# Optimization experiments

Measured on AMD Instinct MI355X. Metric: run time of the kernel, lower is better.

Reference implementation:

```python
import jax, jax.numpy as jnp
import numpy as np

EPS = 1e-12  # matches torch F.normalize default eps
TEMP = 0.1


def _gram(x):
    # L2-normalize rows; for unit vectors 1 - 0.5*||xi-xj||^2 == xi . xj
    n = x / jnp.maximum(jnp.linalg.norm(x, axis=-1, keepdims=True), EPS)
    return n @ n.T  # [N, N]


def setup_inputs() -> dict:
    key = jax.random.key(0)
    k1, k2, k3, k4 = jax.random.split(key, 4)
    N, D = 4096, 512
    return {
        "fm_rgb": jax.random.normal(k1, (N, D), dtype=jnp.float32),
        "fm_depth": jax.random.normal(k2, (N, D), dtype=jnp.float32),
        "fm_ir": jax.random.normal(k3, (N, D), dtype=jnp.float32),
        "fm_t": jax.random.normal(k4, (N, D), dtype=jnp.float32),
    }


def reference(fm_rgb, fm_depth, fm_ir, fm_t):
    G_rgb = _gram(fm_rgb)
    G_depth = _gram(fm_depth)
    G_ir = _gram(fm_ir)
    G_t = _gram(fm_t)
    inv_t = 1.0 / TEMP
    loss_rgb = jnp.mean((G_t * inv_t - G_rgb * inv_t) ** 2)
    loss_depth = jnp.mean((G_t * inv_t - G_depth * inv_t) ** 2)
    loss_ir = jnp.mean((G_t * inv_t - G_ir * inv_t) ** 2)
    return loss_rgb + loss_depth + loss_ir
```

## Files before the change

kernel.cpp:

```cpp
#include <hip/hip_runtime.h>
#include <hip/hip_bf16.h>


typedef __attribute__((ext_vector_type(4))) float floatx4;
typedef __attribute__((ext_vector_type(2))) long long llx2;

#define N_ROWS 4096
#define DDIM   512
#define LOSS_SCALE 9.094947017729282e-11f

__device__ __forceinline__ const float* sel_mod(int mod, const float* a,
                                                const float* b, const float* c,
                                                const float* d) {
  return mod == 0 ? a : mod == 1 ? b : mod == 2 ? c : d;
}

__device__ __forceinline__ float bfr(float x) {
  __hip_bfloat16 h = __float2bfloat16(x);
  unsigned short u = *(unsigned short*)&h;
  return __uint_as_float(((unsigned int)u) << 16);
}

__global__ __launch_bounds__(256) void preprocess_kernel(
    const float* __restrict__ in0, const float* __restrict__ in1,
    const float* __restrict__ in2, const float* __restrict__ in3,
    unsigned char* __restrict__ nT8, float* __restrict__ out) {
  int mod = blockIdx.y;
  int k0 = blockIdx.x * 32;
  const float* X = sel_mod(mod, in0, in1, in2, in3) + (size_t)k0 * DDIM;

  if (blockIdx.x == 0 && blockIdx.y == 0 && threadIdx.x == 0)
    out[0] = 0.f;

  __shared__ float rsc[32];
  __shared__ unsigned int t8[128 * 9];

  int t = threadIdx.x;
  int w = t >> 6, lane = t & 63;

#pragma unroll
  for (int i = 0; i < 8; ++i) {
    int r = w * 8 + i;
    const float4* rp = (const float4*)(X + (size_t)r * DDIM);
    float4 a = rp[lane];
    float4 b = rp[lane + 64];
    float ss = a.x * a.x + a.y * a.y + a.z * a.z + a.w * a.w +
               b.x * b.x + b.y * b.y + b.z * b.z + b.w * b.w;
#pragma unroll
    for (int off = 32; off > 0; off >>= 1) ss += __shfl_down(ss, off, 64);
    if (lane == 0) rsc[r] = 16.0f / fmaxf(sqrtf(ss), 1e-12f);
  }
  __syncthreads();

  int ag = t >> 5;
  int bg = t & 31;
  float sc[4];
#pragma unroll
  for (int q = 0; q < 4; ++q) sc[q] = rsc[ag * 4 + q];

  for (int p = 0; p < 4; ++p) {
    float4 v[4];
#pragma unroll
    for (int q = 0; q < 4; ++q)
      v[q] = ((const float4*)(X + (size_t)(ag * 4 + q) * DDIM + p * 128))[bg];
#pragma unroll
    for (int j = 0; j < 4; ++j) {
      float f0 = bfr(((const float*)&v[0])[j] * sc[0]);
      float f1 = bfr(((const float*)&v[1])[j] * sc[1]);
      float f2 = bfr(((const float*)&v[2])[j] * sc[2]);
      float f3 = bfr(((const float*)&v[3])[j] * sc[3]);
      unsigned int pk = __builtin_amdgcn_cvt_pk_fp8_f32(f0, f1, 0, 0);
      pk = __builtin_amdgcn_cvt_pk_fp8_f32(f2, f3, pk, 1);
      t8[(bg * 4 + j) * 9 + ag] = pk;
    }
    __syncthreads();
    {
      int col = t >> 1, g = t & 1;
      uint4 o;
      o.x = t8[col * 9 + g * 4 + 0];
      o.y = t8[col * 9 + g * 4 + 1];
      o.z = t8[col * 9 + g * 4 + 2];
      o.w = t8[col * 9 + g * 4 + 3];
      *(uint4*)(nT8 + ((size_t)(mod * DDIM + p * 128 + col)) * N_ROWS + k0 +
                g * 16) = o;
    }
    __syncthreads();
  }
}

__device__ __forceinline__ void stage_tiles(
    const unsigned char* __restrict__ Abase,
    const unsigned char* __restrict__ Bbase, int k0,
    unsigned char* ls, int w, int lane) {
  int rr = lane >> 3;
  int s = lane & 7;
#pragma unroll
  for (int c = 0; c < 2; ++c) {
    int base = c * 32 + w * 8;
    int row = base + rr;
    int gc = s ^ ((row >> 1) & 7);
    const unsigned char* ga = Abase + (size_t)row * N_ROWS + k0 + gc * 16;
    __builtin_amdgcn_global_load_lds(
        (__attribute__((address_space(1))) void*)(void*)ga,
        (__attribute__((address_space(3))) void*)(void*)&ls[base * 128],
        16, 0, 0);
  }
#pragma unroll
  for (int c = 0; c < 2; ++c) {
    int base = c * 32 + w * 8;
    int row = base + rr;
    int gc = s ^ ((row >> 1) & 7);
    const unsigned char* gb = Bbase + (size_t)row * N_ROWS + k0 + gc * 16;
    __builtin_amdgcn_global_load_lds(
        (__attribute__((address_space(1))) void*)(void*)gb,
        (__attribute__((address_space(3))) void*)(void*)&ls[8192 + base * 128],
        16, 0, 0);
  }
}

__device__ __forceinline__ void compute_tiles(
    const unsigned char* ls, floatx4 acc[2][2], int wm, int wn, int lm,
    int lq) {
  llx2 A16[2][2], B16[2][2];
#pragma unroll
  for (int mi = 0; mi < 2; ++mi) {
    int row = wm + mi * 16 + lm;
    int sw = (row >> 1) & 7;
    A16[mi][0] = *(const llx2*)&ls[row * 128 + ((lq * 2) ^ sw) * 16];
    A16[mi][1] = *(const llx2*)&ls[row * 128 + ((lq * 2 + 1) ^ sw) * 16];
  }
#pragma unroll
  for (int ni = 0; ni < 2; ++ni) {
    int row = wn + ni * 16 + lm;
    int sw = (row >> 1) & 7;
    B16[ni][0] = *(const llx2*)&ls[8192 + row * 128 + ((lq * 2) ^ sw) * 16];
    B16[ni][1] =
        *(const llx2*)&ls[8192 + row * 128 + ((lq * 2 + 1) ^ sw) * 16];
  }
#pragma unroll
  for (int ks = 0; ks < 4; ++ks) {
    int h = ks >> 1, e = ks & 1;
#pragma unroll
    for (int mi = 0; mi < 2; ++mi)
#pragma unroll
      for (int ni = 0; ni < 2; ++ni)
        acc[mi][ni] = __builtin_amdgcn_mfma_f32_16x16x32_fp8_fp8(
            A16[mi][h][e], B16[ni][h][e], acc[mi][ni], 0, 0, 0);
  }
}

__global__ __launch_bounds__(256) void gram_frob_kernel(
    const unsigned char* __restrict__ nT8, float* __restrict__ out) {
  __shared__ __align__(16) unsigned char ls[2][16384];
  __shared__ float red[4];

  int bx = blockIdx.x;
  int pa_, pb_, ti, tj;
  float wgt;
  if (bx < 144) {
    int p = bx / 36;
    int t36 = bx - p * 36;
    int i = 0;
    while (t36 >= 8 - i) { t36 -= 8 - i; ++i; }
    ti = i;
    tj = i + t36;
    const int   sm[4] = {3, 0, 1, 2};
    const float sw_[4] = {3.f, 1.f, 1.f, 1.f};
    pa_ = sm[p];
    pb_ = sm[p];
    wgt = sw_[p] * (ti == tj ? 1.f : 2.f);
  } else {
    int r = bx - 144;
    int p = r >> 6;
    int t64 = r & 63;
    ti = t64 >> 3;
    tj = t64 & 7;
    pa_ = 3;
    pb_ = p;
    wgt = -2.f;
  }

  int a0 = ti * 64;
  int b0 = tj * 64;
  const unsigned char* Abase = nT8 + ((size_t)pa_ * DDIM + a0) * N_ROWS;
  const unsigned char* Bbase = nT8 + ((size_t)pb_ * DDIM + b0) * N_ROWS;

  int t = threadIdx.x;
  int w = t >> 6;
  int lane = t & 63;
  int wm = (w >> 1) * 32;
  int wn = (w & 1) * 32;
  int lm = lane & 15;
  int lq = lane >> 4;

  floatx4 zero = {0.f, 0.f, 0.f, 0.f};
  floatx4 acc[2][2];
#pragma unroll
  for (int mi = 0; mi < 2; ++mi)
#pragma unroll
    for (int ni = 0; ni < 2; ++ni) acc[mi][ni] = zero;

  stage_tiles(Abase, Bbase, 0, ls[0], w, lane);
  __syncthreads();
  for (int i = 0; i < 15; ++i) {
    int k0 = (2 * i + 1) * 128;
    stage_tiles(Abase, Bbase, k0, ls[1], w, lane);
    compute_tiles(ls[0], acc, wm, wn, lm, lq);
    __syncthreads();
    stage_tiles(Abase, Bbase, k0 + 128, ls[0], w, lane);
    compute_tiles(ls[1], acc, wm, wn, lm, lq);
    __syncthreads();
  }
  stage_tiles(Abase, Bbase, 31 * 128, ls[1], w, lane);
  compute_tiles(ls[0], acc, wm, wn, lm, lq);
  __syncthreads();
  compute_tiles(ls[1], acc, wm, wn, lm, lq);

  float s = 0.f;
#pragma unroll
  for (int mi = 0; mi < 2; ++mi)
#pragma unroll
    for (int ni = 0; ni < 2; ++ni)
#pragma unroll
      for (int r = 0; r < 4; ++r) {
        float v = acc[mi][ni][r];
        s += v * v;
      }
#pragma unroll
  for (int off = 32; off > 0; off >>= 1) s += __shfl_down(s, off, 64);
  if (lane == 0) red[w] = s;
  __syncthreads();
  if (t == 0) {
    float tot = red[0] + red[1] + red[2] + red[3];
    atomicAdd(out, wgt * LOSS_SCALE * tot);
  }
}

extern "C" void kernel_launch(void* const* d_in, const int* in_sizes, int n_in,
                              void* d_out, int out_size, void* d_ws, size_t ws_size,
                              hipStream_t stream) {
  const float* in_rgb   = (const float*)d_in[0];
  const float* in_depth = (const float*)d_in[1];
  const float* in_ir    = (const float*)d_in[2];
  const float* in_t     = (const float*)d_in[3];

  unsigned char* nT8 = (unsigned char*)d_ws;

  preprocess_kernel<<<dim3(128, 4), 256, 0, stream>>>(
      in_rgb, in_depth, in_ir, in_t, nT8, (float*)d_out);
  gram_frob_kernel<<<dim3(336), 256, 0, stream>>>(nT8, (float*)d_out);
}
```

Baseline: 109.9 us.

## Use single-wave GEMM blocks with 4-stage async LDS pipeline and wider preprocess

```diff
diff --git a/kernel.cpp b/kernel.cpp
--- a/kernel.cpp
+++ b/kernel.cpp
@@ -21,138 +21,149 @@
   return __uint_as_float(((unsigned int)u) << 16);
 }
 
-__global__ __launch_bounds__(256) void preprocess_kernel(
+__global__ __launch_bounds__(512) void preprocess_kernel(
     const float* __restrict__ in0, const float* __restrict__ in1,
     const float* __restrict__ in2, const float* __restrict__ in3,
     unsigned char* __restrict__ nT8, float* __restrict__ out) {
   int mod = blockIdx.y;
-  int k0 = blockIdx.x * 32;
+  int k0 = blockIdx.x * 64;
   const float* X = sel_mod(mod, in0, in1, in2, in3) + (size_t)k0 * DDIM;
 
   if (blockIdx.x == 0 && blockIdx.y == 0 && threadIdx.x == 0)
     out[0] = 0.f;
 
-  __shared__ float rsc[32];
-  __shared__ unsigned int t8[128 * 9];
+  __shared__ float rsc[64];
+  __shared__ unsigned int t8[512 * 17];
 
   int t = threadIdx.x;
-  int w = t >> 6, lane = t & 63;
-
-#pragma unroll
-  for (int i = 0; i < 8; ++i) {
-    int r = w * 8 + i;
-    const float4* rp = (const float4*)(X + (size_t)r * DDIM);
-    float4 a = rp[lane];
-    float4 b = rp[lane + 64];
-    float ss = a.x * a.x + a.y * a.y + a.z * a.z + a.w * a.w +
-               b.x * b.x + b.y * b.y + b.z * b.z + b.w * b.w;
-#pragma unroll
-    for (int off = 32; off > 0; off >>= 1) ss += __shfl_down(ss, off, 64);
-    if (lane == 0) rsc[r] = 16.0f / fmaxf(sqrtf(ss), 1e-12f);
+  int a = t >> 5;
+  int bg = t & 31;
+
+  float4 v[4][4];
+#pragma unroll
+  for (int q = 0; q < 4; ++q)
+#pragma unroll
+    for (int p = 0; p < 4; ++p)
+      v[q][p] = ((const float4*)(X + (size_t)(4 * a + q) * DDIM + p * 128))[bg];
+
+  float ss[4];
+#pragma unroll
+  for (int q = 0; q < 4; ++q) {
+    float acc = 0.f;
+#pragma unroll
+    for (int p = 0; p < 4; ++p) {
+      float4 u = v[q][p];
+      acc += u.x * u.x + u.y * u.y + u.z * u.z + u.w * u.w;
+    }
+    ss[q] = acc;
+  }
+#pragma unroll
+  for (int off = 16; off > 0; off >>= 1)
+#pragma unroll
+    for (int q = 0; q < 4; ++q) ss[q] += __shfl_down(ss[q], off, 32);
+  if (bg == 0) {
+#pragma unroll
+    for (int q = 0; q < 4; ++q)
+      rsc[4 * a + q] = 16.0f / fmaxf(sqrtf(ss[q]), 1e-12f);
   }
   __syncthreads();
 
-  int ag = t >> 5;
-  int bg = t & 31;
   float sc[4];
 #pragma unroll
-  for (int q = 0; q < 4; ++q) sc[q] = rsc[ag * 4 + q];
-
-  for (int p = 0; p < 4; ++p) {
-    float4 v[4];
-#pragma unroll
-    for (int q = 0; q < 4; ++q)
-      v[q] = ((const float4*)(X + (size_t)(ag * 4 + q) * DDIM + p * 128))[bg];
+  for (int q = 0; q < 4; ++q) sc[q] = rsc[4 * a + q];
+
+#pragma unroll
+  for (int p = 0; p < 4; ++p)
 #pragma unroll
     for (int j = 0; j < 4; ++j) {
-      float f0 = bfr(((const float*)&v[0])[j] * sc[0]);
-      float f1 = bfr(((const float*)&v[1])[j] * sc[1]);
-      float f2 = bfr(((const float*)&v[2])[j] * sc[2]);
-      float f3 = bfr(((const float*)&v[3])[j] * sc[3]);
+      float f0 = bfr(((const float*)&v[0][p])[j] * sc[0]);
+      float f1 = bfr(((const float*)&v[1][p])[j] * sc[1]);
+      float f2 = bfr(((const float*)&v[2][p])[j] * sc[2]);
+      float f3 = bfr(((const float*)&v[3][p])[j] * sc[3]);
       unsigned int pk = __builtin_amdgcn_cvt_pk_fp8_f32(f0, f1, 0, 0);
       pk = __builtin_amdgcn_cvt_pk_fp8_f32(f2, f3, pk, 1);
-      t8[(bg * 4 + j) * 9 + ag] = pk;
+      t8[(p * 128 + bg * 4 + j) * 17 + a] = pk;
     }
-    __syncthreads();
-    {
-      int col = t >> 1, g = t & 1;
-      uint4 o;
-      o.x = t8[col * 9 + g * 4 + 0];
-      o.y = t8[col * 9 + g * 4 + 1];
-      o.z = t8[col * 9 + g * 4 + 2];
-      o.w = t8[col * 9 + g * 4 + 3];
-      *(uint4*)(nT8 + ((size_t)(mod * DDIM + p * 128 + col)) * N_ROWS + k0 +
-                g * 16) = o;
-    }
-    __syncthreads();
-  }
-}
-
-__device__ __forceinline__ void stage_tiles(
+  __syncthreads();
+
+#pragma unroll
+  for (int it = 0; it < 4; ++it) {
+    int idx = it * 512 + t;
+    int col = idx >> 2;
+    int g = idx & 3;
+    uint4 o;
+    o.x = t8[col * 17 + g * 4 + 0];
+    o.y = t8[col * 17 + g * 4 + 1];
+    o.z = t8[col * 17 + g * 4 + 2];
+    o.w = t8[col * 17 + g * 4 + 3];
+    *(uint4*)(nT8 + ((size_t)(mod * DDIM + col)) * N_ROWS + k0 + g * 16) = o;
+  }
+}
+
+__device__ __forceinline__ void stage_tiles1w(
     const unsigned char* __restrict__ Abase,
     const unsigned char* __restrict__ Bbase, int k0,
-    unsigned char* ls, int w, int lane) {
+    unsigned char* ls, int lane) {
   int rr = lane >> 3;
   int s = lane & 7;
 #pragma unroll
-  for (int c = 0; c < 2; ++c) {
-    int base = c * 32 + w * 8;
-    int row = base + rr;
+  for (int c = 0; c < 8; ++c) {
+    int row = c * 8 + rr;
     int gc = s ^ ((row >> 1) & 7);
     const unsigned char* ga = Abase + (size_t)row * N_ROWS + k0 + gc * 16;
     __builtin_amdgcn_global_load_lds(
         (__attribute__((address_space(1))) void*)(void*)ga,
-        (__attribute__((address_space(3))) void*)(void*)&ls[base * 128],
+        (__attribute__((address_space(3))) void*)(void*)&ls[c * 1024],
         16, 0, 0);
   }
 #pragma unroll
-  for (int c = 0; c < 2; ++c) {
-    int base = c * 32 + w * 8;
-    int row = base + rr;
+  for (int c = 0; c < 8; ++c) {
+    int row = c * 8 + rr;
     int gc = s ^ ((row >> 1) & 7);
     const unsigned char* gb = Bbase + (size_t)row * N_ROWS + k0 + gc * 16;
     __builtin_amdgcn_global_load_lds(
         (__attribute__((address_space(1))) void*)(void*)gb,
-        (__attribute__((address_space(3))) void*)(void*)&ls[8192 + base * 128],
+        (__attribute__((address_space(3))) void*)(void*)&ls[8192 + c * 1024],
         16, 0, 0);
   }
 }
 
-__device__ __forceinline__ void compute_tiles(
-    const unsigned char* ls, floatx4 acc[2][2], int wm, int wn, int lm,
-    int lq) {
-  llx2 A16[2][2], B16[2][2];
-#pragma unroll
-  for (int mi = 0; mi < 2; ++mi) {
-    int row = wm + mi * 16 + lm;
+__device__ __forceinline__ void compute_tiles1w(const unsigned char* ls,
+                                                floatx4 acc[4][4], int lm,
+                                                int lq) {
+  llx2 A16[4][2], B16[4][2];
+#pragma unroll
+  for (int mi = 0; mi < 4; ++mi) {
+    int row = mi * 16 + lm;
     int sw = (row >> 1) & 7;
     A16[mi][0] = *(const llx2*)&ls[row * 128 + ((lq * 2) ^ sw) * 16];
     A16[mi][1] = *(const llx2*)&ls[row * 128 + ((lq * 2 + 1) ^ sw) * 16];
   }
 #pragma unroll
-  for (int ni = 0; ni < 2; ++ni) {
-    int row = wn + ni * 16 + lm;
+  for (int ni = 0; ni < 4; ++ni) {
+    int row = ni * 16 + lm;
     int sw = (row >> 1) & 7;
     B16[ni][0] = *(const llx2*)&ls[8192 + row * 128 + ((lq * 2) ^ sw) * 16];
     B16[ni][1] =
         *(const llx2*)&ls[8192 + row * 128 + ((lq * 2 + 1) ^ sw) * 16];
   }
+  __builtin_amdgcn_s_setprio(1);
 #pragma unroll
   for (int ks = 0; ks < 4; ++ks) {
     int h = ks >> 1, e = ks & 1;
 #pragma unroll
-    for (int mi = 0; mi < 2; ++mi)
-#pragma unroll
-      for (int ni = 0; ni < 2; ++ni)
+    for (int mi = 0; mi < 4; ++mi)
+#pragma unroll
+      for (int ni = 0; ni < 4; ++ni)
         acc[mi][ni] = __builtin_amdgcn_mfma_f32_16x16x32_fp8_fp8(
             A16[mi][h][e], B16[ni][h][e], acc[mi][ni], 0, 0, 0);
   }
-}
-
-__global__ __launch_bounds__(256) void gram_frob_kernel(
+  __builtin_amdgcn_s_setprio(0);
+}
+
+__global__ __launch_bounds__(64) void gram_frob_kernel(
     const unsigned char* __restrict__ nT8, float* __restrict__ out) {
-  __shared__ __align__(16) unsigned char ls[2][16384];
-  __shared__ float red[4];
+  __shared__ __align__(16) unsigned char ls[4][16384];
 
   int bx = blockIdx.x;
   int pa_, pb_, ti, tj;
@@ -180,47 +191,48 @@
     wgt = -2.f;
   }
 
-  int a0 = ti * 64;
-  int b0 = tj * 64;
-  const unsigned char* Abase = nT8 + ((size_t)pa_ * DDIM + a0) * N_ROWS;
-  const unsigned char* Bbase = nT8 + ((size_t)pb_ * DDIM + b0) * N_ROWS;
-
-  int t = threadIdx.x;
-  int w = t >> 6;
-  int lane = t & 63;
-  int wm = (w >> 1) * 32;
-  int wn = (w & 1) * 32;
+  const unsigned char* Abase = nT8 + ((size_t)pa_ * DDIM + ti * 64) * N_ROWS;
+  const unsigned char* Bbase = nT8 + ((size_t)pb_ * DDIM + tj * 64) * N_ROWS;
+
+  int lane = threadIdx.x;
   int lm = lane & 15;
   int lq = lane >> 4;
 
   floatx4 zero = {0.f, 0.f, 0.f, 0.f};
-  floatx4 acc[2][2];
-#pragma unroll
-  for (int mi = 0; mi < 2; ++mi)
-#pragma unroll
-    for (int ni = 0; ni < 2; ++ni) acc[mi][ni] = zero;
-
-  stage_tiles(Abase, Bbase, 0, ls[0], w, lane);
-  __syncthreads();
-  for (int i = 0; i < 15; ++i) {
-    int k0 = (2 * i + 1) * 128;
-    stage_tiles(Abase, Bbase, k0, ls[1], w, lane);
-    compute_tiles(ls[0], acc, wm, wn, lm, lq);
-    __syncthreads();
-    stage_tiles(Abase, Bbase, k0 + 128, ls[0], w, lane);
-    compute_tiles(ls[1], acc, wm, wn, lm, lq);
-    __syncthreads();
-  }
-  stage_tiles(Abase, Bbase, 31 * 128, ls[1], w, lane);
-  compute_tiles(ls[0], acc, wm, wn, lm, lq);
-  __syncthreads();
-  compute_tiles(ls[1], acc, wm, wn, lm, lq);
+  floatx4 acc[4][4];
+#pragma unroll
+  for (int mi = 0; mi < 4; ++mi)
+#pragma unroll
+    for (int ni = 0; ni < 4; ++ni) acc[mi][ni] = zero;
+
+  unsigned char* p0 = ls[0];
+  unsigned char* p1 = ls[1];
+  unsigned char* p2 = ls[2];
+  unsigned char* p3 = ls[3];
+  stage_tiles1w(Abase, Bbase, 0, p0, lane);
+  stage_tiles1w(Abase, Bbase, 128, p1, lane);
+  stage_tiles1w(Abase, Bbase, 256, p2, lane);
+  for (int i = 0; i < 30; ++i) {
+    asm volatile("s_waitcnt vmcnt(32)" ::: "memory");
+    __builtin_amdgcn_sched_barrier(0);
+    if (i < 29)
+      stage_tiles1w(Abase, Bbase, (i + 3) * 128, p3, lane);
+    compute_tiles1w(p0, acc, lm, lq);
+    unsigned char* tmp = p0; p0 = p1; p1 = p2; p2 = p3; p3 = tmp;
+  }
+  asm volatile("s_waitcnt vmcnt(16)" ::: "memory");
+  __builtin_amdgcn_sched_barrier(0);
+  compute_tiles1w(p0, acc, lm, lq);
+  p0 = p1;
+  asm volatile("s_waitcnt vmcnt(0)" ::: "memory");
+  __builtin_amdgcn_sched_barrier(0);
+  compute_tiles1w(p0, acc, lm, lq);
 
   float s = 0.f;
 #pragma unroll
-  for (int mi = 0; mi < 2; ++mi)
-#pragma unroll
-    for (int ni = 0; ni < 2; ++ni)
+  for (int mi = 0; mi < 4; ++mi)
+#pragma unroll
+    for (int ni = 0; ni < 4; ++ni)
 #pragma unroll
       for (int r = 0; r < 4; ++r) {
         float v = acc[mi][ni][r];
@@ -228,12 +240,7 @@
       }
 #pragma unroll
   for (int off = 32; off > 0; off >>= 1) s += __shfl_down(s, off, 64);
-  if (lane == 0) red[w] = s;
-  __syncthreads();
-  if (t == 0) {
-    float tot = red[0] + red[1] + red[2] + red[3];
-    atomicAdd(out, wgt * LOSS_SCALE * tot);
-  }
+  if (lane == 0) atomicAdd(out, wgt * LOSS_SCALE * s);
 }
 
 extern "C" void kernel_launch(void* const* d_in, const int* in_sizes, int n_in,
@@ -246,7 +253,7 @@
 
   unsigned char* nT8 = (unsigned char*)d_ws;
 
-  preprocess_kernel<<<dim3(128, 4), 256, 0, stream>>>(
+  preprocess_kernel<<<dim3(64, 4), 512, 0, stream>>>(
       in_rgb, in_depth, in_ir, in_t, nT8, (float*)d_out);
-  gram_frob_kernel<<<dim3(336), 256, 0, stream>>>(nT8, (float*)d_out);
-}
+  gram_frob_kernel<<<dim3(336), 64, 0, stream>>>(nT8, (float*)d_out);
+}
```

Result: no change. 108.8 us (-1.1%).
